# Kernel tuning notes

Hardware: AMD Instinct MI355X
Metric: run time of the kernel (lower is better)

The kernel has to match this reference:

```python
import jax, jax.numpy as jnp
import numpy as np

B, S, T = 1024, 1024, 32  # batch, seq_len, num_tags


def setup_inputs() -> dict:
    key = jax.random.key(0)
    k1, k2, k3, k4 = jax.random.split(key, 4)
    logits = jax.random.normal(k1, (B, S, T), dtype=jnp.float32)
    transitions = jax.random.normal(k2, (T, T), dtype=jnp.float32)
    tags = jax.random.randint(k3, (B, S), 0, T)
    lengths = jax.random.randint(k4, (B,), 1, S + 1)
    return {"logits": logits, "transitions": transitions, "tags": tags, "lengths": lengths}


def _forward_alg(logits, transitions):
    # viterbi_0 = logits[:, 0, :]; then for t>=1:
    # v_next[b, j] = logsumexp_i(v[b, i] + trans[i, j]) + logits[b, t, j]
    v0 = logits[:, 0, :]  # (B, T)
    emits = jnp.swapaxes(logits[:, 1:, :], 0, 1)  # (S-1, B, T)

    def step(v, emit_t):
        v_next = jax.nn.logsumexp(v[:, :, None] + transitions[None, :, :], axis=1) + emit_t
        return v_next, None

    v_final, _ = jax.lax.scan(step, v0, emits)
    return jax.nn.logsumexp(v_final, axis=1)  # (B,)


def _score_sentence(logits, transitions, tags, lengths):
    # emission scores of gold tags, masked to t < length (note: original ignores
    # lengths in the forward algorithm but uses them here, faithfully reproduced)
    emit = jnp.take_along_axis(logits, tags[:, :, None], axis=2)[..., 0]  # (B, S)
    pos = jnp.arange(S)
    emit_mask = (pos[None, :] < lengths[:, None]).astype(logits.dtype)
    score = jnp.sum(emit * emit_mask, axis=1)
    # transition scores trans[tags[t-1], tags[t]] for 1 <= t < length
    trans_sc = transitions[tags[:, :-1], tags[:, 1:]]  # (B, S-1)
    trans_mask = (pos[None, 1:] < lengths[:, None]).astype(logits.dtype)
    score = score + jnp.sum(trans_sc * trans_mask, axis=1)
    return score  # (B,)


def reference(logits, transitions, tags, lengths):
    log_z = _forward_alg(logits, transitions)
    gold = _score_sentence(logits, transitions, tags, lengths)
    return jnp.mean(log_z - gold)
```

## Files before the change

kernel.cpp:

```cpp
#include <hip/hip_runtime.h>

#define NB 1024
#define NS 1024
#define NT 32
#define L2E 1.44269504088896340736f
#define LN2 0.69314718055994530942f

typedef short        bfrag  __attribute__((ext_vector_type(8)));
typedef float        cfrag  __attribute__((ext_vector_type(16)));
typedef __bf16       bf16x2 __attribute__((ext_vector_type(2)));
typedef float        f32x8  __attribute__((ext_vector_type(8)));
typedef float        f32x4  __attribute__((ext_vector_type(4)));
typedef float        f32x2  __attribute__((ext_vector_type(2)));
typedef unsigned int u32;
typedef unsigned int u32x4  __attribute__((ext_vector_type(4)));

__device__ __forceinline__ float fexp2(float x){ return __builtin_amdgcn_exp2f(x); }
__device__ __forceinline__ float flog2(float x){ return __builtin_amdgcn_logf(x); }

__device__ __forceinline__ u32 pkbf_rne(float a, float b){
    f32x2 t; t.x = a; t.y = b;
    return __builtin_bit_cast(u32, __builtin_convertvector(t, bf16x2));
}
__device__ __forceinline__ u32 pkbf_t(float a, float b){
    return __builtin_amdgcn_perm(__builtin_bit_cast(u32, b),
                                 __builtin_bit_cast(u32, a), 0x07060302u);
}
__device__ __forceinline__ bfrag mk_afrag(f32x8 v){
    u32x4 r;
    r[0] = pkbf_rne(v[0], v[1]); r[1] = pkbf_rne(v[2], v[3]);
    r[2] = pkbf_rne(v[4], v[5]); r[3] = pkbf_rne(v[6], v[7]);
    return __builtin_bit_cast(bfrag, r);
}
__device__ __forceinline__ int exref(float ref){
    u32 xb = __builtin_bit_cast(u32, ref);
    u32 xf = __builtin_amdgcn_readfirstlane(xb);
    int ex = (int)((xf >> 23) & 0xFFu) - 127;
    return ex < -120 ? -120 : (ex > 120 ? 120 : ex);
}

__device__ __forceinline__ int rho(int k){
    int bb = (k >> 2) & 3;
    return (bb == 1 || bb == 2) ? (k ^ 12) : k;
}

template<int N> struct ic { static constexpr int value = N; };
union accu { cfrag c; f32x2 p[8]; };
union q4u  { f32x4 v; f32x2 p[2]; };

#define MFMA(A,B,C) __builtin_amdgcn_mfma_f32_32x32x16_bf16( \
    (A), __builtin_bit_cast(bfrag, B), (C), 0, 0, 0)

__global__ __launch_bounds__(128, 8) void crf_chunk(
    const float* __restrict__ logits, const float* __restrict__ trans,
    const int* __restrict__ tags, const int* __restrict__ lens,
    u32* __restrict__ wmat, float* __restrict__ woff,
    float* __restrict__ gpart, float* __restrict__ outz)
{
    __shared__ __align__(16) float dscall[2 * 512];

    const int tid = threadIdx.x;
    const int wv  = tid >> 6, lt = tid & 63;
    const int m   = lt & 31,  h  = lt >> 5;
    const int bc  = blockIdx.x * 2 + wv;
    const int b   = bc >> 3,  c  = bc & 7;
    float* dsc = dscall + wv * 512;

    if (blockIdx.x == 0 && tid == 0) *outz = 0.0f;

    const float* base = logits + (size_t)b * NS * NT;
    const int    len  = lens[b];
    const int    tb   = b * NS;

    f32x8 Et0, Et1;
    #pragma unroll
    for (int j = 0; j < 8; j++){
        Et0[j] = fexp2(L2E * trans[rho(     8*h + j)*NT + m]);
        Et1[j] = fexp2(L2E * trans[rho(16 + 8*h + j)*NT + m]);
    }
    const bfrag A0f = mk_afrag(Et0);
    const bfrag A1f = mk_afrag(Et1);

    u32x4 B0v, B1v;
    #pragma unroll
    for (int d = 0; d < 4; d++){
        int k0 = 8*h + 2*d;      u32 v = 0;
        if (rho(k0)     == m) v |= 0x3F80u;
        if (rho(k0 + 1) == m) v |= 0x3F800000u;
        B0v[d] = v;
        int k1 = 16 + 8*h + 2*d; v = 0;
        if (rho(k1)     == m) v |= 0x3F80u;
        if (rho(k1 + 1) == m) v |= 0x3F800000u;
        B1v[d] = v;
    }

    cfrag zacc;
    #pragma unroll
    for (int q = 0; q < 16; q++) zacc[q] = 0.0f;

    int   offi = 0;
    float exf  = 0.0f;
    const int tbeg = c*128 + 1;

    float eA[4], eB[4];

    auto issue = [&](float (&e)[4], int k){
        const int t0 = tbeg + k*8 + 4*h;
        #pragma unroll
        for (int i = 0; i < 4; i++){
            int t = t0 + i; t = t > (NS-1) ? (NS-1) : t;
            e[i] = base[t*NT + m];
        }
    };
    auto commit = [&](float (&e)[4], int k){
        float* sp = dsc + (k & 1)*256 + (4*h)*32 + m;
        float a0 = (h == 0) ? -exf : 0.0f;
        sp[0]    = fexp2(fmaf(L2E, e[0], a0));
        sp[32]   = fexp2(L2E * e[1]);
        sp[64]   = fexp2(L2E * e[2]);
        sp[96]   = fexp2(L2E * e[3]);
    };

    auto procN = [&](int k, bool defer, auto nstc){
        constexpr int NST = decltype(nstc)::value;
        const float* db = dsc + (k & 1)*256 + 4*h;
        #pragma unroll
        for (int i = 0; i < NST; i++){
            accu acc;
            acc.c = MFMA(A0f, B0v, zacc);
            acc.c = MFMA(A1f, B1v, acc.c);

            q4u d0, d1, d2, d3;
            d0.v = *(const f32x4*)(db + i*32 +  0);
            d1.v = *(const f32x4*)(db + i*32 +  8);
            d2.v = *(const f32x4*)(db + i*32 + 16);
            d3.v = *(const f32x4*)(db + i*32 + 24);
            acc.p[0] *= d0.p[0]; acc.p[1] *= d0.p[1];
            acc.p[2] *= d1.p[0]; acc.p[3] *= d1.p[1];
            acc.p[4] *= d2.p[0]; acc.p[5] *= d2.p[1];
            acc.p[6] *= d3.p[0]; acc.p[7] *= d3.p[1];

            if (i == 7 && defer){
                int ex = exref(fmaxf(acc.c[0], acc.c[8]));
                offi += ex;
                exf = (float)ex;
            }

            B0v[0] = pkbf_t(acc.c[0],  acc.c[1]);  B0v[1] = pkbf_t(acc.c[2],  acc.c[3]);
            B0v[2] = pkbf_t(acc.c[4],  acc.c[5]);  B0v[3] = pkbf_t(acc.c[6],  acc.c[7]);
            B1v[0] = pkbf_t(acc.c[8],  acc.c[9]);  B1v[1] = pkbf_t(acc.c[10], acc.c[11]);
            B1v[2] = pkbf_t(acc.c[12], acc.c[13]); B1v[3] = pkbf_t(acc.c[14], acc.c[15]);
        }
    };

    issue(eA, 0); commit(eA, 0);
    #pragma unroll 1
    for (int k = 0; k < 14; k += 2){
        issue(eB, k + 1);
        procN(k, true, ic<8>{});
        commit(eB, k + 1);
        issue(eA, k + 2);
        procN(k + 1, true, ic<8>{});
        commit(eA, k + 2);
    }
    issue(eB, 15);
    procN(14, true, ic<8>{});
    commit(eB, 15);
    if (c != 7) procN(15, false, ic<8>{});
    else        procN(15, false, ic<7>{});

    {
        u32* wp = wmat + (size_t)bc * 512 + (size_t)lt * 8;
        *(u32x4*)(wp)     = B0v;
        *(u32x4*)(wp + 4) = B1v;
    }
    if (lt == 0) woff[bc] = (float)offi;

    {
        const int t1 = tbeg + 2*lt;
        const int t2 = t1 + 1;
        const int i2 = t2 > (NS-1) ? (NS-1) : t2;
        const int g0 = tags[tb + t1 - 1];
        const int g1 = tags[tb + t1];
        const int g2 = tags[tb + i2];
        float gg = 0.0f;
        if (t1 < len) gg += base[t1*NT + g1] + trans[g0*NT + g1];
        if (t2 < len) gg += base[t2*NT + g2] + trans[g1*NT + g2];
        #pragma unroll
        for (int d = 1; d < 64; d <<= 1) gg += __shfl_xor(gg, d, 64);
        if (lt == 0){
            if (c == 0) gg += base[tags[tb]];
            gpart[bc] = gg;
        }
    }
}

__global__ __launch_bounds__(256) void crf_combine(
    const float* __restrict__ logits,
    const u32* __restrict__ wmat, const float* __restrict__ woff,
    const float* __restrict__ gpart, float* __restrict__ out)
{
    const int tid = threadIdx.x;
    const int wv  = tid >> 6, lt = tid & 63;
    const int m   = lt & 31,  h  = lt >> 5;
    const int b   = blockIdx.x * 4 + wv;
    const float* base = logits + (size_t)b * NS * NT;

    uint4 mf[16];
    const u32* wb = wmat + (size_t)b * 8 * 512 + (size_t)lt * 8;
    #pragma unroll
    for (int j = 0; j < 8; j++){
        mf[2*j]     = *(const uint4*)(wb + j*512);
        mf[2*j + 1] = *(const uint4*)(wb + j*512 + 4);
    }

    float4 gp0 = ((const float4*)(gpart + b*8))[0];
    float4 gp1 = ((const float4*)(gpart + b*8))[1];
    const float gold = (gp0.x + gp0.y) + (gp0.z + gp0.w)
                     + (gp1.x + gp1.y) + (gp1.z + gp1.w);

    float voff = 0.0f;
    #pragma unroll
    for (int cc = 0; cc < 8; cc++) voff += woff[b*8 + cc];

    u32x4 S0, S1;
    #pragma unroll
    for (int d = 0; d < 4; d++){
        int k0 = 8*h + 2*d;      u32 v = 0;
        if (rho(k0)     == m) v |= 0x3F80u;
        if (rho(k0 + 1) == m) v |= 0x3F800000u;
        S0[d] = v;
        int k1 = 16 + 8*h + 2*d; v = 0;
        if (rho(k1)     == m) v |= 0x3F80u;
        if (rho(k1 + 1) == m) v |= 0x3F800000u;
        S1[d] = v;
    }

    cfrag zacc;
    #pragma unroll
    for (int q = 0; q < 16; q++) zacc[q] = 0.0f;

    #pragma unroll
    for (int j = 7; j >= 0; j--){
        accu acc;
        acc.c = MFMA(__builtin_bit_cast(bfrag, mf[2*j]),     S0, zacc);
        acc.c = MFMA(__builtin_bit_cast(bfrag, mf[2*j + 1]), S1, acc.c);

        float mx = acc.c[0];
        #pragma unroll
        for (int q = 1; q < 16; q++) mx = fmaxf(mx, acc.c[q]);
        #pragma unroll
        for (int d = 1; d < 64; d <<= 1) mx = fmaxf(mx, __shfl_xor(mx, d, 64));
        int ex = exref(mx);
        float sc = __builtin_bit_cast(float, (u32)(127 - ex) << 23);
        #pragma unroll
        for (int q = 0; q < 16; q++) acc.c[q] *= sc;
        voff += (float)ex;

        S0[0] = pkbf_t(acc.c[0],  acc.c[1]);  S0[1] = pkbf_t(acc.c[2],  acc.c[3]);
        S0[2] = pkbf_t(acc.c[4],  acc.c[5]);  S0[3] = pkbf_t(acc.c[6],  acc.c[7]);
        S1[0] = pkbf_t(acc.c[8],  acc.c[9]);  S1[1] = pkbf_t(acc.c[10], acc.c[11]);
        S1[2] = pkbf_t(acc.c[12], acc.c[13]); S1[3] = pkbf_t(acc.c[14], acc.c[15]);
    }

    u32x4 V0, V1;
    #pragma unroll
    for (int d = 0; d < 4; d++){
        int k0 = 8*h + 2*d;
        V0[d] = pkbf_rne(fexp2(L2E * base[rho(k0)]), fexp2(L2E * base[rho(k0+1)]));
        int k1 = 16 + 8*h + 2*d;
        V1[d] = pkbf_rne(fexp2(L2E * base[rho(k1)]), fexp2(L2E * base[rho(k1+1)]));
    }

    accu fin;
    fin.c = MFMA(__builtin_bit_cast(bfrag, S0), V0, zacc);
    fin.c = MFMA(__builtin_bit_cast(bfrag, S1), V1, fin.c);

    float s = 0.0f;
    #pragma unroll
    for (int q = 0; q < 16; q++) s += fin.c[q];
    s += __shfl_xor(s, 32, 64);

    if (lt == 0){
        float logz = LN2 * (voff + flog2(s));
        atomicAdd(out, (logz - gold) * (1.0f / (float)NB));
    }
}

extern "C" void kernel_launch(void* const* d_in, const int* in_sizes, int n_in,
                              void* d_out, int out_size, void* d_ws, size_t ws_size,
                              hipStream_t stream) {
    const float* logits = (const float*)d_in[0];
    const float* trans  = (const float*)d_in[1];
    const int*   tags   = (const int*)d_in[2];
    const int*   lens   = (const int*)d_in[3];

    u32*   wmat  = (u32*)d_ws;
    float* woff  = (float*)((char*)d_ws + 16u*1024u*1024u);
    float* gpart = woff + 8192;

    crf_chunk  <<<4096, 128, 0, stream>>>(logits, trans, tags, lens,
                                          wmat, woff, gpart, (float*)d_out);
    crf_combine<<< 256, 256, 0, stream>>>(logits, wmat, woff, gpart,
                                          (float*)d_out);
}
```

Before: 248.9 us.

## Fold emission scaling into MFMA A-operand, dropping LDS staging of exp(emits)

Measured after the change: 258.5 us. 3.9% more time.

```diff
diff --git a/kernel.cpp b/kernel.cpp
--- a/kernel.cpp
+++ b/kernel.cpp
@@ -26,12 +26,6 @@
     return __builtin_amdgcn_perm(__builtin_bit_cast(u32, b),
                                  __builtin_bit_cast(u32, a), 0x07060302u);
 }
-__device__ __forceinline__ bfrag mk_afrag(f32x8 v){
-    u32x4 r;
-    r[0] = pkbf_rne(v[0], v[1]); r[1] = pkbf_rne(v[2], v[3]);
-    r[2] = pkbf_rne(v[4], v[5]); r[3] = pkbf_rne(v[6], v[7]);
-    return __builtin_bit_cast(bfrag, r);
-}
 __device__ __forceinline__ int exref(float ref){
     u32 xb = __builtin_bit_cast(u32, ref);
     u32 xf = __builtin_amdgcn_readfirstlane(xb);
@@ -46,25 +40,22 @@
 
 template<int N> struct ic { static constexpr int value = N; };
 union accu { cfrag c; f32x2 p[8]; };
-union q4u  { f32x4 v; f32x2 p[2]; };
-
-#define MFMA(A,B,C) __builtin_amdgcn_mfma_f32_32x32x16_bf16( \
-    (A), __builtin_bit_cast(bfrag, B), (C), 0, 0, 0)
-
-__global__ __launch_bounds__(128, 8) void crf_chunk(
+union e8u  { f32x8 v; f32x2 p[4]; };
+
+#define MFMA2(Au, Bu, C) __builtin_amdgcn_mfma_f32_32x32x16_bf16( \
+    __builtin_bit_cast(bfrag, Au), __builtin_bit_cast(bfrag, Bu), (C), 0, 0, 0)
+
+__global__ __launch_bounds__(128, 6) void crf_chunk(
     const float* __restrict__ logits, const float* __restrict__ trans,
     const int* __restrict__ tags, const int* __restrict__ lens,
     u32* __restrict__ wmat, float* __restrict__ woff,
     float* __restrict__ gpart, float* __restrict__ outz)
 {
-    __shared__ __align__(16) float dscall[2 * 512];
-
     const int tid = threadIdx.x;
     const int wv  = tid >> 6, lt = tid & 63;
     const int m   = lt & 31,  h  = lt >> 5;
     const int bc  = blockIdx.x * 2 + wv;
     const int b   = bc >> 3,  c  = bc & 7;
-    float* dsc = dscall + wv * 512;
 
     if (blockIdx.x == 0 && tid == 0) *outz = 0.0f;
 
@@ -72,14 +63,12 @@
     const int    len  = lens[b];
     const int    tb   = b * NS;
 
-    f32x8 Et0, Et1;
+    e8u Et0, Et1;
     #pragma unroll
     for (int j = 0; j < 8; j++){
-        Et0[j] = fexp2(L2E * trans[rho(     8*h + j)*NT + m]);
-        Et1[j] = fexp2(L2E * trans[rho(16 + 8*h + j)*NT + m]);
-    }
-    const bfrag A0f = mk_afrag(Et0);
-    const bfrag A1f = mk_afrag(Et1);
+        Et0.v[j] = fexp2(L2E * trans[rho(     8*h + j)*NT + m]);
+        Et1.v[j] = fexp2(L2E * trans[rho(16 + 8*h + j)*NT + m]);
+    }
 
     u32x4 B0v, B1v;
     #pragma unroll
@@ -102,43 +91,40 @@
     float exf  = 0.0f;
     const int tbeg = c*128 + 1;
 
-    float eA[4], eB[4];
-
-    auto issue = [&](float (&e)[4], int k){
-        const int t0 = tbeg + k*8 + 4*h;
-        #pragma unroll
-        for (int i = 0; i < 4; i++){
+    float eA[8], eB[8];
+
+    auto issue = [&](float (&e)[8], int k){
+        const int t0 = tbeg + k*8;
+        #pragma unroll
+        for (int i = 0; i < 8; i++){
             int t = t0 + i; t = t > (NS-1) ? (NS-1) : t;
             e[i] = base[t*NT + m];
         }
     };
-    auto commit = [&](float (&e)[4], int k){
-        float* sp = dsc + (k & 1)*256 + (4*h)*32 + m;
-        float a0 = (h == 0) ? -exf : 0.0f;
-        sp[0]    = fexp2(fmaf(L2E, e[0], a0));
-        sp[32]   = fexp2(L2E * e[1]);
-        sp[64]   = fexp2(L2E * e[2]);
-        sp[96]   = fexp2(L2E * e[3]);
-    };
-
-    auto procN = [&](int k, bool defer, auto nstc){
+
+    auto procN = [&](float (&e)[8], bool defer, auto nstc){
         constexpr int NST = decltype(nstc)::value;
-        const float* db = dsc + (k & 1)*256 + 4*h;
         #pragma unroll
         for (int i = 0; i < NST; i++){
+            float s = (i == 0) ? fexp2(fmaf(L2E, e[0], -exf))
+                               : fexp2(L2E * e[i]);
+            f32x2 s2; s2.x = s; s2.y = s;
+
+            u32x4 A0p, A1p;
+            {
+                f32x2 r0 = Et0.p[0]*s2, r1 = Et0.p[1]*s2;
+                f32x2 r2 = Et0.p[2]*s2, r3 = Et0.p[3]*s2;
+                A0p[0] = pkbf_t(r0.x, r0.y); A0p[1] = pkbf_t(r1.x, r1.y);
+                A0p[2] = pkbf_t(r2.x, r2.y); A0p[3] = pkbf_t(r3.x, r3.y);
+                f32x2 q0 = Et1.p[0]*s2, q1 = Et1.p[1]*s2;
+                f32x2 q2 = Et1.p[2]*s2, q3 = Et1.p[3]*s2;
+                A1p[0] = pkbf_t(q0.x, q0.y); A1p[1] = pkbf_t(q1.x, q1.y);
+                A1p[2] = pkbf_t(q2.x, q2.y); A1p[3] = pkbf_t(q3.x, q3.y);
+            }
+
             accu acc;
-            acc.c = MFMA(A0f, B0v, zacc);
-            acc.c = MFMA(A1f, B1v, acc.c);
-
-            q4u d0, d1, d2, d3;
-            d0.v = *(const f32x4*)(db + i*32 +  0);
-            d1.v = *(const f32x4*)(db + i*32 +  8);
-            d2.v = *(const f32x4*)(db + i*32 + 16);
-            d3.v = *(const f32x4*)(db + i*32 + 24);
-            acc.p[0] *= d0.p[0]; acc.p[1] *= d0.p[1];
-            acc.p[2] *= d1.p[0]; acc.p[3] *= d1.p[1];
-            acc.p[4] *= d2.p[0]; acc.p[5] *= d2.p[1];
-            acc.p[6] *= d3.p[0]; acc.p[7] *= d3.p[1];
+            acc.c = MFMA2(A0p, B0v, zacc);
+            acc.c = MFMA2(A1p, B1v, acc.c);
 
             if (i == 7 && defer){
                 int ex = exref(fmaxf(acc.c[0], acc.c[8]));
@@ -153,21 +139,18 @@
         }
     };
 
-    issue(eA, 0); commit(eA, 0);
+    issue(eA, 0);
     #pragma unroll 1
     for (int k = 0; k < 14; k += 2){
         issue(eB, k + 1);
-        procN(k, true, ic<8>{});
-        commit(eB, k + 1);
+        procN(eA, true, ic<8>{});
         issue(eA, k + 2);
-        procN(k + 1, true, ic<8>{});
-        commit(eA, k + 2);
+        procN(eB, true, ic<8>{});
     }
     issue(eB, 15);
-    procN(14, true, ic<8>{});
-    commit(eB, 15);
-    if (c != 7) procN(15, false, ic<8>{});
-    else        procN(15, false, ic<7>{});
+    procN(eA, true, ic<8>{});
+    if (c != 7) procN(eB, false, ic<8>{});
+    else        procN(eB, false, ic<7>{});
 
     {
         u32* wp = wmat + (size_t)bc * 512 + (size_t)lt * 8;
@@ -243,8 +226,8 @@
     #pragma unroll
     for (int j = 7; j >= 0; j--){
         accu acc;
-        acc.c = MFMA(__builtin_bit_cast(bfrag, mf[2*j]),     S0, zacc);
-        acc.c = MFMA(__builtin_bit_cast(bfrag, mf[2*j + 1]), S1, acc.c);
+        acc.c = MFMA2(mf[2*j],     S0, zacc);
+        acc.c = MFMA2(mf[2*j + 1], S1, acc.c);
 
         float mx = acc.c[0];
         #pragma unroll
@@ -273,8 +256,8 @@
     }
 
     accu fin;
-    fin.c = MFMA(__builtin_bit_cast(bfrag, S0), V0, zacc);
-    fin.c = MFMA(__builtin_bit_cast(bfrag, S1), V1, fin.c);
+    fin.c = MFMA2(S0, V0, zacc);
+    fin.c = MFMA2(S1, V1, fin.c);
 
     float s = 0.0f;
     #pragma unroll
```
